# Optimization experiments

Hardware: AMD Instinct MI355X
Metric: run time of the kernel (lower is better)

The kernel has to match this reference:

```python
import jax, jax.numpy as jnp
import numpy as np

D = 256       # d_model
HEADS = 8
LEVELS = 3
POINTS = 4
HD = D // HEADS  # head_dim = 32
B, LQ = 32, 300
SHAPES = [(80, 80), (40, 40), (20, 20)]  # (H_l, W_l) per level, 640px / {8,16,32}
LV = sum(h * w for h, w in SHAPES)       # 8400


def setup_inputs() -> dict:
    key = jax.random.key(0)
    ks = jax.random.split(key, 12)
    s = 0.02
    starts = np.cumsum([0] + [h * w for h, w in SHAPES[:-1]])
    return {
        "query": jax.random.normal(ks[0], (B, LQ, D), jnp.float32),
        "reference_points": jax.random.uniform(ks[1], (B, LQ, LEVELS, 4), jnp.float32, 0.05, 0.95),
        "value": jax.random.normal(ks[2], (B, LV, D), jnp.float32),
        "spatial_shapes": jnp.asarray(SHAPES, jnp.int32),
        "level_start_index": jnp.asarray(starts, jnp.int32),
        "Wv": jax.random.normal(ks[3], (D, D), jnp.float32) * s,
        "bv": jnp.zeros((D,), jnp.float32),
        "Woff": jax.random.normal(ks[4], (D, HEADS * LEVELS * POINTS * 2), jnp.float32) * s,
        "boff": jax.random.normal(ks[5], (HEADS * LEVELS * POINTS * 2,), jnp.float32) * 0.5,
        "Wattn": jax.random.normal(ks[6], (D, HEADS * LEVELS * POINTS), jnp.float32) * s,
        "battn": jnp.zeros((HEADS * LEVELS * POINTS,), jnp.float32),
        "Wout": jax.random.normal(ks[7], (D, D), jnp.float32) * s,
        "bout": jnp.zeros((D,), jnp.float32),
    }


def _bilinear_sample(v, loc, Hl, Wl):
    """v: [B, H, Hl*Wl, hd] flattened level feature per head.
    loc: [B, H, N, 2] normalized sampling locations in [0,1] (x, y).
    Matches torch grid_sample(mode=bilinear, padding=zeros, align_corners=False)
    with grid = 2*loc - 1, i.e. pixel coord = loc*size - 0.5."""
    x = loc[..., 0] * Wl - 0.5
    y = loc[..., 1] * Hl - 0.5
    x0f = jnp.floor(x); y0f = jnp.floor(y)
    wx1 = x - x0f; wx0 = 1.0 - wx1
    wy1 = y - y0f; wy0 = 1.0 - wy1
    x0 = x0f.astype(jnp.int32); y0 = y0f.astype(jnp.int32)
    x1 = x0 + 1; y1 = y0 + 1

    def corner(xi, yi):
        valid = ((xi >= 0) & (xi < Wl) & (yi >= 0) & (yi < Hl)).astype(v.dtype)
        idx = jnp.clip(yi, 0, Hl - 1) * Wl + jnp.clip(xi, 0, Wl - 1)
        g = jnp.take_along_axis(v, idx[..., None], axis=2)  # [B,H,N,hd]
        return g * valid[..., None]

    return (wy0[..., None] * (wx0[..., None] * corner(x0, y0) + wx1[..., None] * corner(x1, y0))
          + wy1[..., None] * (wx0[..., None] * corner(x0, y1) + wx1[..., None] * corner(x1, y1)))


def reference(query, reference_points, value, spatial_shapes, level_start_index,
              Wv, bv, Woff, boff, Wattn, battn, Wout, bout):
    Bq, Lq, C = query.shape
    H, L, P, hd = HEADS, LEVELS, POINTS, HD

    v = (value @ Wv + bv).reshape(Bq, -1, H, hd)                       # [B,Lv,H,hd]
    off = (query @ Woff + boff).reshape(Bq, Lq, H, L, P, 2)
    attn = jax.nn.softmax((query @ Wattn + battn).reshape(Bq, Lq, H, L * P), axis=-1)
    attn = attn.reshape(Bq, Lq, H, L, P)

    ref_xy = reference_points[:, :, None, :, None, :2]                 # [B,Lq,1,L,1,2]
    ref_wh = reference_points[:, :, None, :, None, 2:] * 0.5
    loc = ref_xy + off * ref_wh                                        # [B,Lq,H,L,P,2]

    shapes = np.asarray(spatial_shapes)
    starts = np.asarray(level_start_index)
    out = jnp.zeros((Bq, Lq, H, hd), v.dtype)
    for l in range(L):
        Hl, Wl = int(shapes[l, 0]), int(shapes[l, 1])
        s0 = int(starts[l])
        v_l = jnp.transpose(v[:, s0:s0 + Hl * Wl], (0, 2, 1, 3))       # [B,H,HW,hd]
        loc_l = jnp.transpose(loc[:, :, :, l], (0, 2, 1, 3, 4)).reshape(Bq, H, Lq * P, 2)
        sampled = _bilinear_sample(v_l, loc_l, Hl, Wl).reshape(Bq, H, Lq, P, hd)
        w_l = jnp.transpose(attn[:, :, :, l], (0, 2, 1, 3))[..., None]  # [B,H,Lq,P,1]
        out = out + jnp.transpose((sampled * w_l).sum(axis=3), (0, 2, 1, 3))
    return out.reshape(Bq, Lq, C) @ Wout + bout
```

## Files before the change

kernel.cpp:

```cpp
#include <hip/hip_runtime.h>

#define NB   32
#define NLQ  300
#define ND   256
#define NH   8
#define NHD  32
#define NLV  8400
#define MVAL (NB * NLV)
#define MQ   (NB * NLQ)

typedef unsigned short u16b;
typedef __bf16 bf16x8 __attribute__((ext_vector_type(8)));
typedef float  f32x4v __attribute__((ext_vector_type(4)));

__device__ __forceinline__ u16b f2b(float f) {
  union { float f; unsigned u; } x; x.f = f;
  unsigned r = x.u + 0x7fffu + ((x.u >> 16) & 1u);
  return (u16b)(r >> 16);
}
__device__ __forceinline__ float b2f(u16b h) {
  union { float f; unsigned u; } x; x.u = ((unsigned)h) << 16;
  return x.f;
}
__device__ __forceinline__ unsigned pack2(float a, float b) {
  return (unsigned)f2b(a) | ((unsigned)f2b(b) << 16);
}
__device__ __forceinline__ float blo(unsigned u) {
  union { float f; unsigned v; } x; x.v = u << 16; return x.f;
}
__device__ __forceinline__ float bhi(unsigned u) {
  union { float f; unsigned v; } x; x.v = u & 0xffff0000u; return x.f;
}

__global__ void prep_weights(const float* __restrict__ Wv, const float* __restrict__ Woff,
                             const float* __restrict__ Wattn, const float* __restrict__ Wout,
                             u16b* __restrict__ WvT, u16b* __restrict__ WcatH,
                             u16b* __restrict__ WcatL, u16b* __restrict__ WoutT) {
  const int n = blockIdx.x, k = threadIdx.x;
  if (n < 256) {
    WvT [n * 256 + k] = f2b(Wv  [k * 256 + n]);
    WoutT[n * 256 + k] = f2b(Wout[k * 256 + n]);
  } else {
    const int c = n - 256;
    const float f = (c < 192) ? Woff[k * 192 + c] : Wattn[k * 96 + (c - 192)];
    const u16b hi = f2b(f);
    WcatH[c * 256 + k] = hi;
    WcatL[c * 256 + k] = f2b(f - b2f(hi));
  }
}

template <int MODE>
__global__ __launch_bounds__(256, 2) void gemm_k(
    const float* __restrict__ A, const u16b* __restrict__ Bhi,
    const float* __restrict__ bias0, float* __restrict__ outf, u16b* __restrict__ outb) {
  constexpr int BM = (MODE == 0) ? 128 : 32;
  constexpr int BN = 256;
  constexpr int MT = BM / 32;
  constexpr int NT = BN / 32;
  constexpr int STR = 40;

  __shared__ u16b Ah[BM * STR];
  __shared__ u16b Bh[BN * STR];

  const int t = threadIdx.x;
  const int wid = t >> 6, lane = t & 63;
  const int lr = lane & 15, kq = lane >> 4;
  const int wm = wid >> 1, wn = wid & 1;
  const int row0 = blockIdx.x * BM;

  f32x4v acc[MT][NT];
  const f32x4v zero = {0.f, 0.f, 0.f, 0.f};
#pragma unroll
  for (int i = 0; i < MT; ++i)
#pragma unroll
    for (int j = 0; j < NT; ++j) acc[i][j] = zero;

  for (int ks = 0; ks < 8; ++ks) {
    const int k0 = ks * 32;
#pragma unroll
    for (int fi = t * 8; fi < BM * 32; fi += 2048) {
      const int r = fi >> 5, kk = fi & 31;
      const float* src = A + (size_t)(row0 + r) * ND + k0 + kk;
      const float4 u0 = *(const float4*)src;
      const float4 u1 = *(const float4*)(src + 4);
      uint4 hw;
      hw.x = pack2(u0.x, u0.y); hw.y = pack2(u0.z, u0.w);
      hw.z = pack2(u1.x, u1.y); hw.w = pack2(u1.z, u1.w);
      *(uint4*)&Ah[r * STR + kk] = hw;
    }
#pragma unroll
    for (int fi = t * 8; fi < BN * 32; fi += 2048) {
      const int n = fi >> 5, kk = fi & 31;
      *(uint4*)&Bh[n * STR + kk] = *(const uint4*)&Bhi[n * ND + k0 + kk];
    }
    __syncthreads();
    bf16x8 af[MT];
#pragma unroll
    for (int im = 0; im < MT; ++im) {
      const int rr = wm * (BM / 2) + im * 16 + lr;
      af[im] = *(const bf16x8*)&Ah[rr * STR + kq * 8];
    }
#pragma unroll
    for (int in = 0; in < NT; ++in) {
      const int nn = wn * (BN / 2) + in * 16 + lr;
      const bf16x8 bh = *(const bf16x8*)&Bh[nn * STR + kq * 8];
#pragma unroll
      for (int im = 0; im < MT; ++im)
        acc[im][in] = __builtin_amdgcn_mfma_f32_16x16x32_bf16(af[im], bh, acc[im][in], 0, 0, 0);
    }
    __syncthreads();
  }
#pragma unroll
  for (int im = 0; im < MT; ++im) {
    const int grb = row0 + wm * (BM / 2) + im * 16 + kq * 4;
#pragma unroll
    for (int in = 0; in < NT; ++in) {
      const int d = wn * (BN / 2) + in * 16 + lr;
#pragma unroll
      for (int rg = 0; rg < 4; ++rg) {
        const int gr = grb + rg;
        const float val = acc[im][in][rg] + bias0[d];
        if constexpr (MODE == 0) {
          const int b = gr / NLV, pos = gr % NLV;
          const int h = d >> 5, ch = d & 31;
          outb[(((size_t)(b * NH + h)) * NLV + pos) * NHD + ch] = f2b(val);
        } else {
          outf[(size_t)gr * ND + d] = val;
        }
      }
    }
  }
}

__global__ __launch_bounds__(256, 2) void gemm_qh(
    const float* __restrict__ A, const u16b* __restrict__ Bhi, const u16b* __restrict__ Blo,
    const float* __restrict__ boff, const float* __restrict__ battn,
    const float* __restrict__ refp, float* __restrict__ pb) {
  constexpr int BM = 32, BN = 288, NT = 9, STR = 40, RSTR = 289;
  __shared__ __align__(16) char smem[51200];
  u16b* Ah = (u16b*)smem;
  u16b* Al = (u16b*)(smem + 2560);
  u16b* Bh = (u16b*)(smem + 5120);
  u16b* Bl = (u16b*)(smem + 28160);
  float* raw = (float*)(smem + 5120);

  const int t = threadIdx.x;
  const int wid = t >> 6, lane = t & 63;
  const int lr = lane & 15, kq = lane >> 4;
  const int wm = wid >> 1, wn = wid & 1;
  const int row0 = blockIdx.x * BM;

  f32x4v acc[NT];
  const f32x4v zero = {0.f, 0.f, 0.f, 0.f};
#pragma unroll
  for (int j = 0; j < NT; ++j) acc[j] = zero;

  for (int ks = 0; ks < 8; ++ks) {
    const int k0 = ks * 32;
    if (t < 128) {
      const int fi = t * 8;
      const int r = fi >> 5, kk = fi & 31;
      const float* src = A + (size_t)(row0 + r) * ND + k0 + kk;
      const float4 u0 = *(const float4*)src;
      const float4 u1 = *(const float4*)(src + 4);
      const float vv[8] = {u0.x, u0.y, u0.z, u0.w, u1.x, u1.y, u1.z, u1.w};
      uint4 hw;
      hw.x = pack2(vv[0], vv[1]); hw.y = pack2(vv[2], vv[3]);
      hw.z = pack2(vv[4], vv[5]); hw.w = pack2(vv[6], vv[7]);
      *(uint4*)&Ah[r * STR + kk] = hw;
      float lo[8];
#pragma unroll
      for (int j = 0; j < 8; ++j) lo[j] = vv[j] - b2f(f2b(vv[j]));
      uint4 lw;
      lw.x = pack2(lo[0], lo[1]); lw.y = pack2(lo[2], lo[3]);
      lw.z = pack2(lo[4], lo[5]); lw.w = pack2(lo[6], lo[7]);
      *(uint4*)&Al[r * STR + kk] = lw;
    }
#pragma unroll
    for (int fi = t * 8; fi < BN * 32; fi += 2048) {
      const int n = fi >> 5, kk = fi & 31;
      *(uint4*)&Bh[n * STR + kk] = *(const uint4*)&Bhi[n * ND + k0 + kk];
      *(uint4*)&Bl[n * STR + kk] = *(const uint4*)&Blo[n * ND + k0 + kk];
    }
    __syncthreads();
    const int rr = wm * 16 + lr;
    const bf16x8 af  = *(const bf16x8*)&Ah[rr * STR + kq * 8];
    const bf16x8 alf = *(const bf16x8*)&Al[rr * STR + kq * 8];
#pragma unroll
    for (int in = 0; in < NT; ++in) {
      const int nn = wn * 144 + in * 16 + lr;
      const bf16x8 bh = *(const bf16x8*)&Bh[nn * STR + kq * 8];
      const bf16x8 bl = *(const bf16x8*)&Bl[nn * STR + kq * 8];
      acc[in] = __builtin_amdgcn_mfma_f32_16x16x32_bf16(af,  bh, acc[in], 0, 0, 0);
      acc[in] = __builtin_amdgcn_mfma_f32_16x16x32_bf16(alf, bh, acc[in], 0, 0, 0);
      acc[in] = __builtin_amdgcn_mfma_f32_16x16x32_bf16(af,  bl, acc[in], 0, 0, 0);
    }
    __syncthreads();
  }
#pragma unroll
  for (int in = 0; in < NT; ++in) {
    const int d = wn * 144 + in * 16 + lr;
    const float bias = (d < 192) ? boff[d] : battn[d - 192];
#pragma unroll
    for (int rg = 0; rg < 4; ++rg) {
      const int row = wm * 16 + kq * 4 + rg;
      raw[row * RSTR + d] = acc[in][rg] + bias;
    }
  }
  __syncthreads();
  {
    const int q = t >> 3, h = t & 7;
    const int gq = row0 + q;
    const float* r = raw + q * RSTR;
    float lg[12], mx = -1e30f;
#pragma unroll
    for (int j = 0; j < 12; ++j) { lg[j] = r[192 + h * 12 + j]; mx = fmaxf(mx, lg[j]); }
    float s = 0.f;
#pragma unroll
    for (int j = 0; j < 12; ++j) { lg[j] = __expf(lg[j] - mx); s += lg[j]; }
    const float inv = 1.f / s;
    float* po = pb + (size_t)gq * 288;
#pragma unroll
    for (int j = 0; j < 12; ++j) po[192 + h * 12 + j] = lg[j] * inv;
    const float* rp = refp + (size_t)gq * 12;
#pragma unroll
    for (int l = 0; l < 3; ++l) {
      const float cx = rp[l * 4 + 0], cy = rp[l * 4 + 1];
      const float wx = rp[l * 4 + 2] * 0.5f, wy = rp[l * 4 + 3] * 0.5f;
#pragma unroll
      for (int p = 0; p < 4; ++p) {
        const float ox = r[h * 24 + (l * 4 + p) * 2 + 0];
        const float oy = r[h * 24 + (l * 4 + p) * 2 + 1];
        po[(h * 12 + l * 4 + p) * 2 + 0] = cx + ox * wx;
        po[(h * 12 + l * 4 + p) * 2 + 1] = cy + oy * wy;
      }
    }
  }
}

__global__ __launch_bounds__(256) void msda_sample(
    const u16b* __restrict__ Vws, const float* __restrict__ pb,
    float* __restrict__ oattn) {
  const int gq0 = blockIdx.x * 4;
  const int t = threadIdx.x;
  __shared__ float spb[4 * 288];
  for (int i = t; i < 4 * 288; i += 256) spb[i] = pb[(size_t)gq0 * 288 + i];
  __syncthreads();
  const int wave = t >> 6, lane = t & 63;
  const int h = lane >> 3, c4 = lane & 7;
  const int gq = gq0 + wave;
  const int b = gq / NLQ;
  const float* P = spb + wave * 288;
  const u16b* vb = Vws + ((size_t)(b * NH + h) * NLV) * NHD + c4 * 4;
  const int WLS[3] = {80, 40, 20};
  const int S0S[3] = {0, 6400, 8000};
  float4 acc = {0.f, 0.f, 0.f, 0.f};
#pragma unroll
  for (int l = 0; l < 3; ++l) {
    const int Wl = WLS[l], s0 = S0S[l];
    const float Wf = (float)Wl;
#pragma unroll
    for (int p = 0; p < 4; ++p) {
      const int si = h * 12 + l * 4 + p;
      const float aw = P[192 + si];
      const float fx = P[si * 2 + 0] * Wf - 0.5f;
      const float fy = P[si * 2 + 1] * Wf - 0.5f;
      const float x0f = floorf(fx), y0f = floorf(fy);
      const float wx1 = fx - x0f, wx0 = 1.f - wx1;
      const float wy1 = fy - y0f, wy0 = 1.f - wy1;
      const int ix = (int)x0f, iy = (int)y0f;
      const float ax0 = ((unsigned)ix < (unsigned)Wl) ? wx0 : 0.f;
      const float ax1 = ((unsigned)(ix + 1) < (unsigned)Wl) ? wx1 : 0.f;
      const float ay0 = ((unsigned)iy < (unsigned)Wl) ? aw * wy0 : 0.f;
      const float ay1 = ((unsigned)(iy + 1) < (unsigned)Wl) ? aw * wy1 : 0.f;
      const int cx0 = min(max(ix, 0), Wl - 1);
      const int cx1 = min(max(ix + 1, 0), Wl - 1);
      const int cy0 = min(max(iy, 0), Wl - 1);
      const int cy1 = min(max(iy + 1, 0), Wl - 1);
      const int r0 = s0 + cy0 * Wl, r1 = s0 + cy1 * Wl;
      const uint2 u00 = *(const uint2*)(vb + (size_t)(r0 + cx0) * NHD);
      const uint2 u10 = *(const uint2*)(vb + (size_t)(r0 + cx1) * NHD);
      const uint2 u01 = *(const uint2*)(vb + (size_t)(r1 + cx0) * NHD);
      const uint2 u11 = *(const uint2*)(vb + (size_t)(r1 + cx1) * NHD);
      const float w00 = ay0 * ax0, w10 = ay0 * ax1;
      const float w01 = ay1 * ax0, w11 = ay1 * ax1;
      acc.x = fmaf(w00, blo(u00.x), acc.x); acc.y = fmaf(w00, bhi(u00.x), acc.y);
      acc.z = fmaf(w00, blo(u00.y), acc.z); acc.w = fmaf(w00, bhi(u00.y), acc.w);
      acc.x = fmaf(w10, blo(u10.x), acc.x); acc.y = fmaf(w10, bhi(u10.x), acc.y);
      acc.z = fmaf(w10, blo(u10.y), acc.z); acc.w = fmaf(w10, bhi(u10.y), acc.w);
      acc.x = fmaf(w01, blo(u01.x), acc.x); acc.y = fmaf(w01, bhi(u01.x), acc.y);
      acc.z = fmaf(w01, blo(u01.y), acc.z); acc.w = fmaf(w01, bhi(u01.y), acc.w);
      acc.x = fmaf(w11, blo(u11.x), acc.x); acc.y = fmaf(w11, bhi(u11.x), acc.y);
      acc.z = fmaf(w11, blo(u11.y), acc.z); acc.w = fmaf(w11, bhi(u11.y), acc.w);
    }
  }
  *(float4*)(oattn + (size_t)gq * ND + h * NHD + c4 * 4) = acc;
}

extern "C" void kernel_launch(void* const* d_in, const int* in_sizes, int n_in,
                              void* d_out, int out_size, void* d_ws, size_t ws_size,
                              hipStream_t stream) {
  (void)in_sizes; (void)n_in; (void)out_size; (void)ws_size;
  const float* query = (const float*)d_in[0];
  const float* refp  = (const float*)d_in[1];
  const float* value = (const float*)d_in[2];
  const float* Wv    = (const float*)d_in[5];
  const float* bv    = (const float*)d_in[6];
  const float* Woff  = (const float*)d_in[7];
  const float* boff  = (const float*)d_in[8];
  const float* Wattn = (const float*)d_in[9];
  const float* battn = (const float*)d_in[10];
  const float* Wout  = (const float*)d_in[11];
  const float* bout  = (const float*)d_in[12];
  float* out = (float*)d_out;

  char* w = (char*)d_ws;
  u16b*  v_ws  = (u16b*)w;  w += (size_t)MVAL * ND * 2;
  u16b*  WvT   = (u16b*)w;  w += (size_t)256 * 256 * 2;
  u16b*  WoutT = (u16b*)w;  w += (size_t)256 * 256 * 2;
  u16b*  WcatH = (u16b*)w;  w += (size_t)288 * 256 * 2;
  u16b*  WcatL = (u16b*)w;  w += (size_t)288 * 256 * 2;
  float* pb    = (float*)w; w += (size_t)MQ * 288 * 4;
  float* oattn = (float*)w; w += (size_t)MQ * ND * 4;

  prep_weights<<<544, 256, 0, stream>>>(Wv, Woff, Wattn, Wout, WvT, WcatH, WcatL, WoutT);
  gemm_k<0><<<MVAL / 128, 256, 0, stream>>>(value, WvT, bv, nullptr, v_ws);
  gemm_qh<<<MQ / 32, 256, 0, stream>>>(query, WcatH, WcatL, boff, battn, refp, pb);
  msda_sample<<<MQ / 4, 256, 0, stream>>>(v_ws, pb, oattn);
  gemm_k<2><<<MQ / 32, 256, 0, stream>>>(oattn, WoutT, bout, out, nullptr);
}
```

Measured before the change: 543.6 us.

## Make value GEMM persistent with resident weights; split query/output GEMMs over N

The value projection becomes a persistent kernel with 256 blocks of 512 threads. Each block loads the full transposed Wv into LDS once, loops over row chunks, and prefetches the next chunk's fp32 activations into registers while the MFMAs run. This removes the repeated per-K-step weight staging and barrier syncs that the tiled GEMM had. The query-head and output GEMMs are also split along N (3 and 2 slices) with smaller LDS footprints and higher occupancy to expose more parallelism, at the cost of re-reading the A tiles for every slice.

```diff
diff --git a/kernel.cpp b/kernel.cpp
--- a/kernel.cpp
+++ b/kernel.cpp
@@ -8,6 +8,7 @@
 #define NLV  8400
 #define MVAL (NB * NLV)
 #define MQ   (NB * NLQ)
+#define NCHUNK (MVAL / 128)
 
 typedef unsigned short u16b;
 typedef __bf16 bf16x8 __attribute__((ext_vector_type(8)));
@@ -49,111 +50,117 @@
   }
 }
 
-template <int MODE>
-__global__ __launch_bounds__(256, 2) void gemm_k(
-    const float* __restrict__ A, const u16b* __restrict__ Bhi,
-    const float* __restrict__ bias0, float* __restrict__ outf, u16b* __restrict__ outb) {
-  constexpr int BM = (MODE == 0) ? 128 : 32;
-  constexpr int BN = 256;
-  constexpr int MT = BM / 32;
-  constexpr int NT = BN / 32;
-  constexpr int STR = 40;
-
-  __shared__ u16b Ah[BM * STR];
-  __shared__ u16b Bh[BN * STR];
+__global__ __launch_bounds__(512, 2) void gemm_v(
+    const float* __restrict__ A, const u16b* __restrict__ WvT,
+    const float* __restrict__ bv, u16b* __restrict__ outb) {
+  __shared__ u16b Bs[256 * 264];
+
+  const int t = threadIdx.x;
+#pragma unroll
+  for (int i = 0; i < 16; ++i) {
+    const int c = i * 512 + t;
+    const int n = c >> 5, kg = c & 31;
+    *(uint4*)&Bs[n * 264 + kg * 8] = *(const uint4*)&WvT[n * 256 + kg * 8];
+  }
+  __syncthreads();
+
+  const int w = t >> 6, lane = t & 63;
+  const int lr = lane & 15, kq = lane >> 4;
+
+  float bias_r[16];
+#pragma unroll
+  for (int in = 0; in < 16; ++in) bias_r[in] = bv[in * 16 + lr];
+
+  f32x4v acc[16];
+  const f32x4v zero = {0.f, 0.f, 0.f, 0.f};
+#pragma unroll
+  for (int in = 0; in < 16; ++in) acc[in] = zero;
+
+  float4 abuf[16];
+  int c = blockIdx.x;
+  {
+    const float* ap = A + (size_t)(c * 128 + w * 16 + lr) * ND + kq * 8;
+#pragma unroll
+    for (int ks = 0; ks < 8; ++ks) {
+      abuf[2 * ks]     = *(const float4*)(ap + ks * 32);
+      abuf[2 * ks + 1] = *(const float4*)(ap + ks * 32 + 4);
+    }
+  }
+
+  while (true) {
+    union { uint4 u; bf16x8 v; } afrag[8];
+#pragma unroll
+    for (int ks = 0; ks < 8; ++ks) {
+      const float4 u0 = abuf[2 * ks], u1 = abuf[2 * ks + 1];
+      afrag[ks].u.x = pack2(u0.x, u0.y); afrag[ks].u.y = pack2(u0.z, u0.w);
+      afrag[ks].u.z = pack2(u1.x, u1.y); afrag[ks].u.w = pack2(u1.z, u1.w);
+    }
+    const int cn = c + 256;
+    const bool more = (cn < NCHUNK);
+    if (more) {
+      const float* ap = A + (size_t)(cn * 128 + w * 16 + lr) * ND + kq * 8;
+#pragma unroll
+      for (int ks = 0; ks < 8; ++ks) {
+        abuf[2 * ks]     = *(const float4*)(ap + ks * 32);
+        abuf[2 * ks + 1] = *(const float4*)(ap + ks * 32 + 4);
+      }
+    }
+#pragma unroll
+    for (int ks = 0; ks < 8; ++ks) {
+      const int kb = ks * 32 + kq * 8;
+#pragma unroll
+      for (int in = 0; in < 16; ++in) {
+        const bf16x8 bf = *(const bf16x8*)&Bs[(in * 16 + lr) * 264 + kb];
+        acc[in] = __builtin_amdgcn_mfma_f32_16x16x32_bf16(afrag[ks].v, bf, acc[in], 0, 0, 0);
+      }
+    }
+    const int row0 = c * 128;
+    const int b0 = row0 / NLV;
+    const int rem0 = row0 - b0 * NLV;
+    const int offw = w * 16 + kq * 4;
+#pragma unroll
+    for (int rg = 0; rg < 4; ++rg) {
+      int pos = rem0 + offw + rg;
+      int b = b0;
+      if (pos >= NLV) { pos -= NLV; b++; }
+#pragma unroll
+      for (int in = 0; in < 16; ++in) {
+        const int h = in >> 1, ch = (in & 1) * 16 + lr;
+        outb[(((size_t)(b * NH + h)) * NLV + pos) * NHD + ch] = f2b(acc[in][rg] + bias_r[in]);
+        acc[in][rg] = 0.f;
+      }
+    }
+    if (!more) break;
+    c = cn;
+  }
+}
+
+__global__ __launch_bounds__(256, 4) void gemm_qh3(
+    const float* __restrict__ A, const u16b* __restrict__ Bhi, const u16b* __restrict__ Blo,
+    const float* __restrict__ boff, const float* __restrict__ battn,
+    const float* __restrict__ refp, float* __restrict__ pb) {
+  constexpr int STR = 40, RSTR = 97;
+  __shared__ __align__(16) char smem[20480];
+  u16b* Ah = (u16b*)smem;
+  u16b* Al = (u16b*)(smem + 2560);
+  u16b* Bh = (u16b*)(smem + 5120);
+  u16b* Bl = (u16b*)(smem + 12800);
+  float* raw = (float*)(smem + 5120);
+
+  const int slice = blockIdx.x % 3;
+  const int mch   = blockIdx.x / 3;
+  const int N0 = slice * 96;
+  const int row0 = mch * 32;
 
   const int t = threadIdx.x;
   const int wid = t >> 6, lane = t & 63;
   const int lr = lane & 15, kq = lane >> 4;
-  const int wm = wid >> 1, wn = wid & 1;
-  const int row0 = blockIdx.x * BM;
-
-  f32x4v acc[MT][NT];
+  const int wm = wid & 1, wn = wid >> 1;
+
+  f32x4v acc[3];
   const f32x4v zero = {0.f, 0.f, 0.f, 0.f};
 #pragma unroll
-  for (int i = 0; i < MT; ++i)
-#pragma unroll
-    for (int j = 0; j < NT; ++j) acc[i][j] = zero;
-
-  for (int ks = 0; ks < 8; ++ks) {
-    const int k0 = ks * 32;
-#pragma unroll
-    for (int fi = t * 8; fi < BM * 32; fi += 2048) {
-      const int r = fi >> 5, kk = fi & 31;
-      const float* src = A + (size_t)(row0 + r) * ND + k0 + kk;
-      const float4 u0 = *(const float4*)src;
-      const float4 u1 = *(const float4*)(src + 4);
-      uint4 hw;
-      hw.x = pack2(u0.x, u0.y); hw.y = pack2(u0.z, u0.w);
-      hw.z = pack2(u1.x, u1.y); hw.w = pack2(u1.z, u1.w);
-      *(uint4*)&Ah[r * STR + kk] = hw;
-    }
-#pragma unroll
-    for (int fi = t * 8; fi < BN * 32; fi += 2048) {
-      const int n = fi >> 5, kk = fi & 31;
-      *(uint4*)&Bh[n * STR + kk] = *(const uint4*)&Bhi[n * ND + k0 + kk];
-    }
-    __syncthreads();
-    bf16x8 af[MT];
-#pragma unroll
-    for (int im = 0; im < MT; ++im) {
-      const int rr = wm * (BM / 2) + im * 16 + lr;
-      af[im] = *(const bf16x8*)&Ah[rr * STR + kq * 8];
-    }
-#pragma unroll
-    for (int in = 0; in < NT; ++in) {
-      const int nn = wn * (BN / 2) + in * 16 + lr;
-      const bf16x8 bh = *(const bf16x8*)&Bh[nn * STR + kq * 8];
-#pragma unroll
-      for (int im = 0; im < MT; ++im)
-        acc[im][in] = __builtin_amdgcn_mfma_f32_16x16x32_bf16(af[im], bh, acc[im][in], 0, 0, 0);
-    }
-    __syncthreads();
-  }
-#pragma unroll
-  for (int im = 0; im < MT; ++im) {
-    const int grb = row0 + wm * (BM / 2) + im * 16 + kq * 4;
-#pragma unroll
-    for (int in = 0; in < NT; ++in) {
-      const int d = wn * (BN / 2) + in * 16 + lr;
-#pragma unroll
-      for (int rg = 0; rg < 4; ++rg) {
-        const int gr = grb + rg;
-        const float val = acc[im][in][rg] + bias0[d];
-        if constexpr (MODE == 0) {
-          const int b = gr / NLV, pos = gr % NLV;
-          const int h = d >> 5, ch = d & 31;
-          outb[(((size_t)(b * NH + h)) * NLV + pos) * NHD + ch] = f2b(val);
-        } else {
-          outf[(size_t)gr * ND + d] = val;
-        }
-      }
-    }
-  }
-}
-
-__global__ __launch_bounds__(256, 2) void gemm_qh(
-    const float* __restrict__ A, const u16b* __restrict__ Bhi, const u16b* __restrict__ Blo,
-    const float* __restrict__ boff, const float* __restrict__ battn,
-    const float* __restrict__ refp, float* __restrict__ pb) {
-  constexpr int BM = 32, BN = 288, NT = 9, STR = 40, RSTR = 289;
-  __shared__ __align__(16) char smem[51200];
-  u16b* Ah = (u16b*)smem;
-  u16b* Al = (u16b*)(smem + 2560);
-  u16b* Bh = (u16b*)(smem + 5120);
-  u16b* Bl = (u16b*)(smem + 28160);
-  float* raw = (float*)(smem + 5120);
-
-  const int t = threadIdx.x;
-  const int wid = t >> 6, lane = t & 63;
-  const int lr = lane & 15, kq = lane >> 4;
-  const int wm = wid >> 1, wn = wid & 1;
-  const int row0 = blockIdx.x * BM;
-
-  f32x4v acc[NT];
-  const f32x4v zero = {0.f, 0.f, 0.f, 0.f};
-#pragma unroll
-  for (int j = 0; j < NT; ++j) acc[j] = zero;
+  for (int j = 0; j < 3; ++j) acc[j] = zero;
 
   for (int ks = 0; ks < 8; ++ks) {
     const int k0 = ks * 32;
@@ -177,18 +184,18 @@
       *(uint4*)&Al[r * STR + kk] = lw;
     }
 #pragma unroll
-    for (int fi = t * 8; fi < BN * 32; fi += 2048) {
+    for (int fi = t * 8; fi < 96 * 32; fi += 2048) {
       const int n = fi >> 5, kk = fi & 31;
-      *(uint4*)&Bh[n * STR + kk] = *(const uint4*)&Bhi[n * ND + k0 + kk];
-      *(uint4*)&Bl[n * STR + kk] = *(const uint4*)&Blo[n * ND + k0 + kk];
+      *(uint4*)&Bh[n * STR + kk] = *(const uint4*)&Bhi[(N0 + n) * ND + k0 + kk];
+      *(uint4*)&Bl[n * STR + kk] = *(const uint4*)&Blo[(N0 + n) * ND + k0 + kk];
     }
     __syncthreads();
     const int rr = wm * 16 + lr;
     const bf16x8 af  = *(const bf16x8*)&Ah[rr * STR + kq * 8];
     const bf16x8 alf = *(const bf16x8*)&Al[rr * STR + kq * 8];
 #pragma unroll
-    for (int in = 0; in < NT; ++in) {
-      const int nn = wn * 144 + in * 16 + lr;
+    for (int in = 0; in < 3; ++in) {
+      const int nn = wn * 48 + in * 16 + lr;
       const bf16x8 bh = *(const bf16x8*)&Bh[nn * STR + kq * 8];
       const bf16x8 bl = *(const bf16x8*)&Bl[nn * STR + kq * 8];
       acc[in] = __builtin_amdgcn_mfma_f32_16x16x32_bf16(af,  bh, acc[in], 0, 0, 0);
@@ -198,43 +205,45 @@
     __syncthreads();
   }
 #pragma unroll
-  for (int in = 0; in < NT; ++in) {
-    const int d = wn * 144 + in * 16 + lr;
-    const float bias = (d < 192) ? boff[d] : battn[d - 192];
+  for (int in = 0; in < 3; ++in) {
+    const int dl = wn * 48 + in * 16 + lr;
+    const int gd = N0 + dl;
+    const float bias = (gd < 192) ? boff[gd] : battn[gd - 192];
 #pragma unroll
     for (int rg = 0; rg < 4; ++rg) {
       const int row = wm * 16 + kq * 4 + rg;
-      raw[row * RSTR + d] = acc[in][rg] + bias;
+      raw[row * RSTR + dl] = acc[in][rg] + bias;
     }
   }
   __syncthreads();
-  {
-    const int q = t >> 3, h = t & 7;
-    const int gq = row0 + q;
-    const float* r = raw + q * RSTR;
+  const int q = t >> 3, gq = row0 + q;
+  if (slice < 2) {
+    const int j6 = t & 7;
+    const float* rp = refp + (size_t)gq * 12;
+    float* po = pb + (size_t)gq * 288;
+#pragma unroll
+    for (int e = 0; e < 6; ++e) {
+      const int sl = j6 * 6 + e;
+      const int si = slice * 48 + sl;
+      const int l = (si % 12) >> 2;
+      const float ox = raw[q * RSTR + sl * 2 + 0];
+      const float oy = raw[q * RSTR + sl * 2 + 1];
+      po[si * 2 + 0] = rp[l * 4 + 0] + ox * rp[l * 4 + 2] * 0.5f;
+      po[si * 2 + 1] = rp[l * 4 + 1] + oy * rp[l * 4 + 3] * 0.5f;
+    }
+  } else {
+    const int h = t & 7;
+    const float* r = raw + q * RSTR + h * 12;
     float lg[12], mx = -1e30f;
 #pragma unroll
-    for (int j = 0; j < 12; ++j) { lg[j] = r[192 + h * 12 + j]; mx = fmaxf(mx, lg[j]); }
+    for (int j = 0; j < 12; ++j) { lg[j] = r[j]; mx = fmaxf(mx, lg[j]); }
     float s = 0.f;
 #pragma unroll
     for (int j = 0; j < 12; ++j) { lg[j] = __expf(lg[j] - mx); s += lg[j]; }
     const float inv = 1.f / s;
-    float* po = pb + (size_t)gq * 288;
-#pragma unroll
-    for (int j = 0; j < 12; ++j) po[192 + h * 12 + j] = lg[j] * inv;
-    const float* rp = refp + (size_t)gq * 12;
-#pragma unroll
-    for (int l = 0; l < 3; ++l) {
-      const float cx = rp[l * 4 + 0], cy = rp[l * 4 + 1];
-      const float wx = rp[l * 4 + 2] * 0.5f, wy = rp[l * 4 + 3] * 0.5f;
-#pragma unroll
-      for (int p = 0; p < 4; ++p) {
-        const float ox = r[h * 24 + (l * 4 + p) * 2 + 0];
-        const float oy = r[h * 24 + (l * 4 + p) * 2 + 1];
-        po[(h * 12 + l * 4 + p) * 2 + 0] = cx + ox * wx;
-        po[(h * 12 + l * 4 + p) * 2 + 1] = cy + oy * wy;
-      }
-    }
+    float* po = pb + (size_t)gq * 288 + 192 + h * 12;
+#pragma unroll
+    for (int j = 0; j < 12; ++j) po[j] = lg[j] * inv;
   }
 }
 
@@ -297,6 +306,69 @@
   *(float4*)(oattn + (size_t)gq * ND + h * NHD + c4 * 4) = acc;
 }
 
+__global__ __launch_bounds__(256, 4) void gemm_out(
+    const float* __restrict__ A, const u16b* __restrict__ Bhi,
+    const float* __restrict__ bias0, float* __restrict__ outf) {
+  constexpr int STR = 40;
+  __shared__ u16b Ah[32 * STR];
+  __shared__ u16b Bh[128 * STR];
+
+  const int slice = blockIdx.x & 1;
+  const int mch   = blockIdx.x >> 1;
+  const int N0 = slice * 128;
+  const int row0 = mch * 32;
+
+  const int t = threadIdx.x;
+  const int wid = t >> 6, lane = t & 63;
+  const int lr = lane & 15, kq = lane >> 4;
+  const int wm = wid & 1, wn = wid >> 1;
+
+  f32x4v acc[4];
+  const f32x4v zero = {0.f, 0.f, 0.f, 0.f};
+#pragma unroll
+  for (int j = 0; j < 4; ++j) acc[j] = zero;
+
+  for (int ks = 0; ks < 8; ++ks) {
+    const int k0 = ks * 32;
+    if (t < 128) {
+      const int fi = t * 8;
+      const int r = fi >> 5, kk = fi & 31;
+      const float* src = A + (size_t)(row0 + r) * ND + k0 + kk;
+      const float4 u0 = *(const float4*)src;
+      const float4 u1 = *(const float4*)(src + 4);
+      uint4 hw;
+      hw.x = pack2(u0.x, u0.y); hw.y = pack2(u0.z, u0.w);
+      hw.z = pack2(u1.x, u1.y); hw.w = pack2(u1.z, u1.w);
+      *(uint4*)&Ah[r * STR + kk] = hw;
+    }
+#pragma unroll
+    for (int fi = t * 8; fi < 128 * 32; fi += 2048) {
+      const int n = fi >> 5, kk = fi & 31;
+      *(uint4*)&Bh[n * STR + kk] = *(const uint4*)&Bhi[(N0 + n) * ND + k0 + kk];
+    }
+    __syncthreads();
+    const int rr = wm * 16 + lr;
+    const bf16x8 af = *(const bf16x8*)&Ah[rr * STR + kq * 8];
+#pragma unroll
+    for (int in = 0; in < 4; ++in) {
+      const int nn = wn * 64 + in * 16 + lr;
+      const bf16x8 bh = *(const bf16x8*)&Bh[nn * STR + kq * 8];
+      acc[in] = __builtin_amdgcn_mfma_f32_16x16x32_bf16(af, bh, acc[in], 0, 0, 0);
+    }
+    __syncthreads();
+  }
+#pragma unroll
+  for (int in = 0; in < 4; ++in) {
+    const int d = N0 + wn * 64 + in * 16 + lr;
+    const float bias = bias0[d];
+#pragma unroll
+    for (int rg = 0; rg < 4; ++rg) {
+      const int gr = row0 + wm * 16 + kq * 4 + rg;
+      outf[(size_t)gr * ND + d] = acc[in][rg] + bias;
+    }
+  }
+}
+
 extern "C" void kernel_launch(void* const* d_in, const int* in_sizes, int n_in,
                               void* d_out, int out_size, void* d_ws, size_t ws_size,
                               hipStream_t stream) {
@@ -324,8 +396,8 @@
   float* oattn = (float*)w; w += (size_t)MQ * ND * 4;
 
   prep_weights<<<544, 256, 0, stream>>>(Wv, Woff, Wattn, Wout, WvT, WcatH, WcatL, WoutT);
-  gemm_k<0><<<MVAL / 128, 256, 0, stream>>>(value, WvT, bv, nullptr, v_ws);
-  gemm_qh<<<MQ / 32, 256, 0, stream>>>(query, WcatH, WcatL, boff, battn, refp, pb);
-  msda_sample<<<MQ / 4, 256, 0, stream>>>(v_ws, pb, oattn);
-  gemm_k<2><<<MQ / 32, 256, 0, stream>>>(oattn, WoutT, bout, out, nullptr);
-}
+  gemm_v<<<256, 512, 0, stream>>>(value, WvT, bv, v_ws);
+  gemm_qh3<<<900, 256, 0, stream>>>(query, WcatH, WcatL, boff, battn, refp, pb);
+  msda_sample<<<2400, 256, 0, stream>>>(v_ws, pb, oattn);
+  gemm_out<<<600, 256, 0, stream>>>(oattn, WoutT, bout, out);
+}
```

Measured after the change: 946.8 us. +74.2%, slower.
